# Kernel tuning notes

Hardware: AMD Instinct MI355X
Metric: run time of the kernel (lower is better)

## Reference

```python
import jax, jax.numpy as jnp
import numpy as np

MAXU = 6          # init arg maxU
MAXV = 6          # init arg maxV (ratio=None)
TRUNC = 4         # cfg.TRUNCATED_SIZE; cfg.TRUNCATED=True, cfg.FLOW_REG_BY_MAX=True


def setup_inputs() -> dict:
    key = jax.random.key(0)
    B, H, W = 8, 128, 160
    U, V = 2 * MAXU + 1, 2 * MAXV + 1
    x = jax.random.normal(key, (B, 1, U, V, H, W), dtype=jnp.float32)
    return {"x": x}


def reference(x):
    # x: [B,1,U,V,H,W] cost volume
    x = x[:, 0]                                   # [B,U,V,H,W]
    b, u, v, h, w = x.shape

    # --- truncation mask (cfg.TRUNCATED) ---
    # argmax over flattened (u,v); scatter one-hot + MaxPool3d((2t+1,2t+1,1))
    # is equivalent to a +-t box around the per-pixel argmax location.
    idx = jnp.argmax(x.reshape(b, u * v, h, w), axis=1)   # [B,H,W] int
    ui = (idx // v)[:, None, None]                        # [B,1,1,H,W]
    vi = (idx % v)[:, None, None]
    ugrid = jnp.arange(u).reshape(1, u, 1, 1, 1)
    vgrid = jnp.arange(v).reshape(1, 1, v, 1, 1)
    mask = (jnp.abs(ugrid - ui) <= TRUNC) & (jnp.abs(vgrid - vi) <= TRUNC)
    xm = jnp.where(mask, x, -jnp.inf)

    # --- softmax over the U*V displacement hypotheses (FLOW_REG_BY_MAX) ---
    p = jax.nn.softmax(xm.reshape(b, u * v, h, w), axis=1).reshape(b, u, v, h, w)

    dispU = jnp.arange(-MAXU, MAXU + 1, dtype=x.dtype)    # [U]
    dispV = jnp.arange(-MAXV, MAXV + 1, dtype=x.dtype)    # [V]
    flowU = jnp.einsum('buvhw,u->bhw', p, dispU)
    flowV = jnp.einsum('buvhw,v->bhw', p, dispV)
    return jnp.stack((flowU, flowV), axis=1)              # [B,2,H,W]
```

## Files before the change

### kernel.cpp

```cpp
#include <hip/hip_runtime.h>
#include <math.h>

#define Bsz 8
#define Udim 13
#define Vdim 13
#define Hdim 128
#define Wdim 160
#define HW (Hdim * Wdim)
#define UV (Udim * Vdim)
#define TRUNC 4
#define NPIX (Bsz * HW)

__global__ __launch_bounds__(256, 2) void flow_regression_kernel(
    const float* __restrict__ x, float* __restrict__ out) {
    int p = blockIdx.x * 256 + threadIdx.x;
    int b  = p / HW;
    int hw = p - b * HW;

    const float* base = x + (size_t)b * UV * HW + hw;

    float vals[UV];
    #pragma unroll
    for (int i = 0; i < UV; ++i) {
        vals[i] = base[(size_t)i * HW];
    }

    float m = vals[0];
    int mi = 0;
    #pragma unroll
    for (int i = 1; i < UV; ++i) {
        if (vals[i] > m) { m = vals[i]; mi = i; }
    }
    int ui = mi / Vdim;
    int vi = mi - ui * Vdim;

    float sum = 0.f, wu = 0.f, wv = 0.f;
    #pragma unroll
    for (int u = 0; u < Udim; ++u) {
        bool uin = (u - ui <= TRUNC) && (ui - u <= TRUNC);
        float rsum = 0.f, rwv = 0.f;
        #pragma unroll
        for (int v = 0; v < Vdim; ++v) {
            float val = vals[u * Vdim + v];
            bool vin = (v - vi <= TRUNC) && (vi - v <= TRUNC);
            float e = vin ? __expf(val - m) : 0.f;
            rsum += e;
            rwv  += e * (float)(v - 6);
        }
        if (uin) {
            sum += rsum;
            wu  += rsum * (float)(u - 6);
            wv  += rwv;
        }
    }
    float inv = 1.0f / sum;
    float* ob = out + (size_t)b * 2 * HW + hw;
    ob[0]  = wu * inv;
    ob[HW] = wv * inv;
}

extern "C" void kernel_launch(void* const* d_in, const int* in_sizes, int n_in,
                              void* d_out, int out_size, void* d_ws, size_t ws_size,
                              hipStream_t stream) {
    const float* x = (const float*)d_in[0];
    float* out = (float*)d_out;
    flow_regression_kernel<<<NPIX / 256, 256, 0, stream>>>(x, out);
}
```

Baseline: 158.1 us.

## Split displacement hypotheses across four wavefronts per pixel with LDS reduction

```diff
diff --git a/kernel.cpp b/kernel.cpp
--- a/kernel.cpp
+++ b/kernel.cpp
@@ -10,53 +10,81 @@
 #define UV (Udim * Vdim)
 #define TRUNC 4
 #define NPIX (Bsz * HW)
+#define NG 4
+#define PPG 43
+#define PIXB 64
 
-__global__ __launch_bounds__(256, 2) void flow_regression_kernel(
+__global__ __launch_bounds__(256, 4) void flow_regression_kernel(
     const float* __restrict__ x, float* __restrict__ out) {
-    int p = blockIdx.x * 256 + threadIdx.x;
-    int b  = p / HW;
-    int hw = p - b * HW;
+    const int lane = threadIdx.x & 63;
+    const int g    = threadIdx.x >> 6;
+    const int p    = blockIdx.x * PIXB + lane;
+    const int b    = p / HW;
+    const int hw   = p - b * HW;
+    const int lo   = g * PPG;
 
-    const float* base = x + (size_t)b * UV * HW + hw;
+    const float* base = x + (size_t)b * UV * HW + (size_t)lo * HW + hw;
 
-    float vals[UV];
+    float vals[PPG];
     #pragma unroll
-    for (int i = 0; i < UV; ++i) {
-        vals[i] = base[(size_t)i * HW];
+    for (int j = 0; j < PPG; ++j) {
+        vals[j] = (lo + j < UV) ? base[(size_t)j * HW] : -INFINITY;
     }
 
-    float m = vals[0];
-    int mi = 0;
+    float m  = vals[0];
+    int   mi = lo;
     #pragma unroll
-    for (int i = 1; i < UV; ++i) {
-        if (vals[i] > m) { m = vals[i]; mi = i; }
+    for (int j = 1; j < PPG; ++j) {
+        if (vals[j] > m) { m = vals[j]; mi = lo + j; }
     }
-    int ui = mi / Vdim;
-    int vi = mi - ui * Vdim;
+
+    __shared__ float sM[NG][PIXB];
+    __shared__ int   sI[NG][PIXB];
+    __shared__ float sS[NG][PIXB], sU[NG][PIXB], sV[NG][PIXB];
+
+    sM[g][lane] = m;
+    sI[g][lane] = mi;
+    __syncthreads();
+
+    float gm  = sM[0][lane];
+    int   gmi = sI[0][lane];
+    #pragma unroll
+    for (int q = 1; q < NG; ++q) {
+        float mq = sM[q][lane];
+        int   iq = sI[q][lane];
+        if (mq > gm) { gm = mq; gmi = iq; }
+    }
+    const int ui = gmi / Vdim;
+    const int vi = gmi - ui * Vdim;
 
     float sum = 0.f, wu = 0.f, wv = 0.f;
+    int u = lo / Vdim;
+    int v = lo - u * Vdim;
     #pragma unroll
-    for (int u = 0; u < Udim; ++u) {
-        bool uin = (u - ui <= TRUNC) && (ui - u <= TRUNC);
-        float rsum = 0.f, rwv = 0.f;
-        #pragma unroll
-        for (int v = 0; v < Vdim; ++v) {
-            float val = vals[u * Vdim + v];
-            bool vin = (v - vi <= TRUNC) && (vi - v <= TRUNC);
-            float e = vin ? __expf(val - m) : 0.f;
-            rsum += e;
-            rwv  += e * (float)(v - 6);
-        }
-        if (uin) {
-            sum += rsum;
-            wu  += rsum * (float)(u - 6);
-            wv  += rwv;
-        }
+    for (int j = 0; j < PPG; ++j) {
+        bool in = (u - ui <= TRUNC) && (ui - u <= TRUNC) &&
+                  (v - vi <= TRUNC) && (vi - v <= TRUNC);
+        float e = in ? __expf(vals[j] - gm) : 0.f;
+        sum += e;
+        wu  += e * (float)(u - 6);
+        wv  += e * (float)(v - 6);
+        if (++v == Vdim) { v = 0; ++u; }
     }
-    float inv = 1.0f / sum;
-    float* ob = out + (size_t)b * 2 * HW + hw;
-    ob[0]  = wu * inv;
-    ob[HW] = wv * inv;
+
+    sS[g][lane] = sum;
+    sU[g][lane] = wu;
+    sV[g][lane] = wv;
+    __syncthreads();
+
+    if (g == 0) {
+        float S = sS[0][lane] + sS[1][lane] + sS[2][lane] + sS[3][lane];
+        float U = sU[0][lane] + sU[1][lane] + sU[2][lane] + sU[3][lane];
+        float V = sV[0][lane] + sV[1][lane] + sV[2][lane] + sV[3][lane];
+        float inv = 1.0f / S;
+        float* ob = out + (size_t)b * 2 * HW + hw;
+        ob[0]  = U * inv;
+        ob[HW] = V * inv;
+    }
 }
 
 extern "C" void kernel_launch(void* const* d_in, const int* in_sizes, int n_in,
@@ -64,5 +92,5 @@
                               hipStream_t stream) {
     const float* x = (const float*)d_in[0];
     float* out = (float*)d_out;
-    flow_regression_kernel<<<NPIX / 256, 256, 0, stream>>>(x, out);
+    flow_regression_kernel<<<NPIX / PIXB, 256, 0, stream>>>(x, out);
 }
```

Result: slower. 163.7 us (+3.5%).
